# Kernel tuning notes

Hardware: AMD Instinct MI355X
Metric: run time of the kernel (lower is better)

The kernel has to match this reference:

```python
import jax, jax.numpy as jnp
import numpy as np

D_MODEL, N_HEADS, LATENT, ROPE = 4096, 128, 512, 64
HEAD_DIM = D_MODEL // N_HEADS  # 32
B, S = 2, 1024


def setup_inputs() -> dict:
    key = jax.random.key(0)
    ks = jax.random.split(key, 9)
    def w(k, i, o):
        return jax.random.normal(k, (i, o), dtype=jnp.float32) * (1.0 / np.sqrt(i))
    return {
        "x": jax.random.normal(ks[0], (B, S, D_MODEL), dtype=jnp.float32),
        "Wq_down": w(ks[1], D_MODEL, LATENT),
        "Wq_up": w(ks[2], LATENT, N_HEADS * HEAD_DIM),
        "Wq_rope": w(ks[3], D_MODEL, N_HEADS * ROPE),
        "Wkv_down": w(ks[4], D_MODEL, LATENT),
        "Wk_up": w(ks[5], LATENT, N_HEADS * HEAD_DIM),
        "Wv_up": w(ks[6], LATENT, N_HEADS * HEAD_DIM),
        "Wk_rope": w(ks[7], D_MODEL, ROPE),
        "Wo": w(ks[8], N_HEADS * HEAD_DIM, D_MODEL),
    }


def reference(x, Wq_down, Wq_up, Wq_rope, Wkv_down, Wk_up, Wv_up, Wk_rope, Wo):
    b, s, _ = x.shape
    # latent down-projections
    c_q = x @ Wq_down                                   # [B,S,latent]
    c_kv = x @ Wkv_down                                 # [B,S,latent]
    # up-projections, reshaped to per-head
    q_c = (c_q @ Wq_up).reshape(b, s, N_HEADS, HEAD_DIM)    # [B,S,H,Dh]
    q_r = (x @ Wq_rope).reshape(b, s, N_HEADS, ROPE)        # [B,S,H,Dr]
    k_c = (c_kv @ Wk_up).reshape(b, s, N_HEADS, HEAD_DIM)   # [B,S,H,Dh]
    v_c = (c_kv @ Wv_up).reshape(b, s, N_HEADS, HEAD_DIM)   # [B,S,H,Dh]
    k_r = x @ Wk_rope                                       # [B,S,Dr] shared over heads
    scale = jnp.asarray((HEAD_DIM + ROPE) ** 0.5, x.dtype)
    # scores = q.k with q=[q_c|q_r], k=[k_c|k_r(broadcast)] -> split the dot product
    scores = (jnp.einsum("bqhd,bkhd->bhqk", q_c, k_c)
              + jnp.einsum("bqhd,bkd->bhqk", q_r, k_r)) / scale  # [B,H,S,S]
    attn = jax.nn.softmax(scores, axis=-1)
    out = jnp.einsum("bhqk,bkhd->bqhd", attn, v_c)          # [B,S,H,Dh]
    out = out.reshape(b, s, N_HEADS * HEAD_DIM)
    return out @ Wo                                         # [B,S,d_model]
```

## Files before the change

kernel.cpp:

```cpp
#include <hip/hip_runtime.h>
#include <hip/hip_bf16.h>
#include <math.h>

#define D_MODEL 4096
#define N_HEADS 128
#define LATENT  512
#define ROPE_D  64
#define HEAD_D  32
#define BATCH   2
#define SEQ     1024
#define NTOK    (BATCH*SEQ)

typedef unsigned short u16;
typedef __attribute__((ext_vector_type(8))) short bf16x8;
typedef __attribute__((ext_vector_type(4))) float f32x4;

__device__ __forceinline__ u16 f2bf(float f) {
    union { float f; unsigned u; } v; v.f = f;
    unsigned r = (v.u + 0x7fffu + ((v.u >> 16) & 1u)) >> 16;
    return (u16)r;
}

__device__ __forceinline__ void gl_lds16(const u16* g, u16* l) {
    __builtin_amdgcn_global_load_lds(
        (const __attribute__((address_space(1))) unsigned int*)g,
        (__attribute__((address_space(3))) unsigned int*)l, 16, 0, 0);
}

__global__ __launch_bounds__(256)
void cast_x_kernel(const float* __restrict__ in, u16* __restrict__ out)
{
    size_t i = ((size_t)blockIdx.x * 256 + threadIdx.x) * 8;
    float4 a = *(const float4*)(in + i);
    float4 b = *(const float4*)(in + i + 4);
    u16 o[8] = {f2bf(a.x), f2bf(a.y), f2bf(a.z), f2bf(a.w),
                f2bf(b.x), f2bf(b.y), f2bf(b.z), f2bf(b.w)};
    *(bf16x8*)(out + i) = *(bf16x8*)o;
}

__global__ __launch_bounds__(256)
void castT_kernel(const float* __restrict__ W, u16* __restrict__ Wt,
                  int K, int N)
{
    __shared__ float tile[32][33];
    const int tid = threadIdx.x;
    const int j0 = blockIdx.x * 32;
    const int i0 = blockIdx.y * 32;
    #pragma unroll
    for (int it = 0; it < 4; ++it) {
        int e = tid + it * 256;
        int r = e >> 5, c = e & 31;
        tile[r][c] = (j0 + c < N) ? W[(size_t)(i0 + r) * N + j0 + c] : 0.f;
    }
    __syncthreads();
    #pragma unroll
    for (int it = 0; it < 4; ++it) {
        int e = tid + it * 256;
        int n = e >> 5, k = e & 31;
        Wt[(size_t)(j0 + n) * K + i0 + k] = f2bf(tile[k][n]);
    }
}

template<int OUTF32>
__global__ __launch_bounds__(256)
void gemm_bf16(const u16* __restrict__ A, const u16* __restrict__ Bt,
               void* __restrict__ Cout, int M, int N, int K,
               int lda, int ldb, int ldc)
{
    __shared__ __align__(16) u16 As[128 * 64];
    __shared__ __align__(16) u16 Bs[128 * 64];

    const int tid  = threadIdx.x;
    const int lane = tid & 63;
    const int wave = tid >> 6;
    const int wr = wave >> 1, wc = wave & 1;
    const int nwg  = gridDim.x * gridDim.y;
    const int orig = blockIdx.y * gridDim.x + blockIdx.x;
    const int swz  = (orig & 7) * (nwg >> 3) + (orig >> 3);
    const int bm = (swz / gridDim.x) * 128, bn = (swz % gridDim.x) * 128;
    const int l15 = lane & 15, lg = lane >> 4;

    f32x4 acc[4][4];
    #pragma unroll
    for (int i = 0; i < 4; ++i)
        #pragma unroll
        for (int j = 0; j < 4; ++j) acc[i][j] = (f32x4){0.f, 0.f, 0.f, 0.f};

    for (int kt = 0; kt < K; kt += 64) {
        __syncthreads();
        #pragma unroll
        for (int i = 0; i < 4; ++i) {
            int f = i * 256 + tid;
            int row = f >> 3, c = f & 7;
            int sc = c ^ (row & 7);
            gl_lds16(A + (size_t)(bm + row) * lda + kt + sc * 8, As + f * 8);
        }
        #pragma unroll
        for (int i = 0; i < 4; ++i) {
            int f = i * 256 + tid;
            int row = f >> 3, c = f & 7;
            int sc = c ^ (row & 7);
            gl_lds16(Bt + (size_t)(bn + row) * ldb + kt + sc * 8, Bs + f * 8);
        }
        __syncthreads();

        #pragma unroll
        for (int t = 0; t < 2; ++t) {
            bf16x8 af[4], bf[4];
            #pragma unroll
            for (int fm = 0; fm < 4; ++fm) {
                int row = wr * 64 + fm * 16 + l15;
                int c = (t * 4 + lg) ^ (row & 7);
                af[fm] = *(const bf16x8*)(As + row * 64 + c * 8);
            }
            #pragma unroll
            for (int fn = 0; fn < 4; ++fn) {
                int row = wc * 64 + fn * 16 + l15;
                int c = (t * 4 + lg) ^ (row & 7);
                bf[fn] = *(const bf16x8*)(Bs + row * 64 + c * 8);
            }
            #pragma unroll
            for (int fm = 0; fm < 4; ++fm)
                #pragma unroll
                for (int fn = 0; fn < 4; ++fn)
                    acc[fm][fn] = __builtin_amdgcn_mfma_f32_16x16x32_bf16(
                        af[fm], bf[fn], acc[fm][fn], 0, 0, 0);
        }
    }

    #pragma unroll
    for (int fm = 0; fm < 4; ++fm)
        #pragma unroll
        for (int fn = 0; fn < 4; ++fn)
            #pragma unroll
            for (int ri = 0; ri < 4; ++ri) {
                int row = bm + wr * 64 + fm * 16 + 4 * lg + ri;
                int col = bn + wc * 64 + fn * 16 + l15;
                if (col < N) {
                    float v = acc[fm][fn][ri];
                    if (OUTF32) ((float*)Cout)[(size_t)row * ldc + col] = v;
                    else        ((u16*)Cout)[(size_t)row * ldc + col] = f2bf(v);
                }
            }
}

__global__ __launch_bounds__(256)
void vtrans_kernel(const u16* __restrict__ vc, u16* __restrict__ vt)
{
    __shared__ __align__(16) u16 tile[64][72];
    const int tid = threadIdx.x;
    const int c0 = blockIdx.x * 64;
    const int s0 = blockIdx.y * 64;
    const int b  = blockIdx.z;
    #pragma unroll
    for (int it = 0; it < 2; ++it) {
        int e = it * 256 + tid;
        int r = e >> 3, c8 = e & 7;
        *(bf16x8*)&tile[r][c8 * 8] =
            *(const bf16x8*)(vc + (size_t)(b * SEQ + s0 + r) * 8192 + c0 + c8 * 8);
    }
    __syncthreads();
    #pragma unroll
    for (int it = 0; it < 2; ++it) {
        int e = it * 256 + tid;
        int d = e >> 3, c8 = e & 7;
        u16 o[8];
        #pragma unroll
        for (int j = 0; j < 8; ++j) o[j] = tile[c8 * 8 + j][d];
        *(bf16x8*)(vt + (size_t)(b * D_MODEL + c0 + d) * SEQ + s0 + c8 * 8) = *(bf16x8*)o;
    }
}

__global__ __launch_bounds__(256)
void attn_kernel(const u16* __restrict__ q_c, const u16* __restrict__ q_r,
                 const u16* __restrict__ k_c, const u16* __restrict__ k_r,
                 const u16* __restrict__ vt,  u16* __restrict__ attn_out)
{
    __shared__ __align__(16) u16 s_kc[2][64 * 32];
    __shared__ __align__(16) u16 s_kr[2][64 * 64];
    __shared__ __align__(16) u16 s_vt[2][32 * 64];
    __shared__ __align__(16) u16 s_p[4][16 * 64];

    const int tid  = threadIdx.x;
    const int lane = tid & 63;
    const int w    = tid >> 6;
    const int l15  = lane & 15, lg = lane >> 4;
    const int q0 = blockIdx.x * 64;
    const int h  = blockIdx.y;
    const int b  = blockIdx.z;
    const size_t bS = (size_t)b * SEQ;
    const int hc = h * HEAD_D;
    const float c2 = 0.1020620726159658f * 1.44269504088896f;

    const int qrow = q0 + w * 16 + l15;
    const bf16x8 qf0 = *(const bf16x8*)(q_c + (bS + qrow) * 4096 + hc + lg * 8);
    const bf16x8 qf1 = *(const bf16x8*)(q_r + (bS + qrow) * 9344 + h * ROPE_D + lg * 8);
    const bf16x8 qf2 = *(const bf16x8*)(q_r + (bS + qrow) * 9344 + h * ROPE_D + 32 + lg * 8);

    float m2 = -1e30f, lsum = 0.f;
    f32x4 oacc[2];
    oacc[0] = (f32x4){0.f, 0.f, 0.f, 0.f};
    oacc[1] = (f32x4){0.f, 0.f, 0.f, 0.f};

    auto stage = [&](int buf, int k0) {
        { int f = tid, r = f >> 2, c = f & 3;
          gl_lds16(k_c + (bS + k0 + r) * 8192 + hc + ((c ^ (r & 3)) << 3),
                   &s_kc[buf][f * 8]); }
        #pragma unroll
        for (int it = 0; it < 2; ++it) {
          int f = it * 256 + tid, r = f >> 3, c = f & 7;
          gl_lds16(k_r + (bS + k0 + r) * 9344 + ((c ^ (r & 7)) << 3),
                   &s_kr[buf][f * 8]); }
        { int f = tid, d = f >> 3, c = f & 7;
          gl_lds16(vt + ((size_t)b * D_MODEL + hc + d) * SEQ + k0 + ((c ^ (d & 7)) << 3),
                   &s_vt[buf][f * 8]); }
    };

    stage(0, 0);
    __syncthreads();

    int cur = 0;
    for (int t = 0; t < SEQ / 64; ++t) {
        if (t + 1 < SEQ / 64) stage(cur ^ 1, (t + 1) * 64);

        f32x4 sc[4];
        #pragma unroll
        for (int fc = 0; fc < 4; ++fc) sc[fc] = (f32x4){0.f, 0.f, 0.f, 0.f};
        __builtin_amdgcn_s_setprio(1);
        #pragma unroll
        for (int fc = 0; fc < 4; ++fc) {
            int row = fc * 16 + l15;
            bf16x8 kb = *(const bf16x8*)&s_kc[cur][row * 32 + ((lg ^ (row & 3)) << 3)];
            sc[fc] = __builtin_amdgcn_mfma_f32_16x16x32_bf16(kb, qf0, sc[fc], 0, 0, 0);
        }
        #pragma unroll
        for (int tt = 0; tt < 2; ++tt) {
            bf16x8 qf = tt ? qf2 : qf1;
            #pragma unroll
            for (int fc = 0; fc < 4; ++fc) {
                int row = fc * 16 + l15;
                bf16x8 kb = *(const bf16x8*)&s_kr[cur][row * 64 + (((tt * 4 + lg) ^ (row & 7)) << 3)];
                sc[fc] = __builtin_amdgcn_mfma_f32_16x16x32_bf16(kb, qf, sc[fc], 0, 0, 0);
            }
        }
        __builtin_amdgcn_s_setprio(0);

        float tmx = sc[0][0];
        #pragma unroll
        for (int fc = 0; fc < 4; ++fc)
            #pragma unroll
            for (int ri = 0; ri < 4; ++ri)
                tmx = fmaxf(tmx, sc[fc][ri]);
        tmx = fmaxf(tmx, __shfl_xor(tmx, 16));
        tmx = fmaxf(tmx, __shfl_xor(tmx, 32));
        float tl2 = tmx * c2;
        if (!__all(tl2 <= m2 + 8.f)) {
            float mn = fmaxf(m2, tl2);
            float corr = exp2f(m2 - mn);
            m2 = mn;
            lsum *= corr;
            #pragma unroll
            for (int ri = 0; ri < 4; ++ri) {
                float cr = __shfl(corr, 4 * lg + ri);
                oacc[0][ri] *= cr; oacc[1][ri] *= cr;
            }
        }
        float rs = 0.f;
        unsigned pk0[4], pk1[4];
        #pragma unroll
        for (int fc = 0; fc < 4; ++fc) {
            float p0 = exp2f(fmaf(sc[fc][0], c2, -m2));
            float p1 = exp2f(fmaf(sc[fc][1], c2, -m2));
            float p2 = exp2f(fmaf(sc[fc][2], c2, -m2));
            float p3 = exp2f(fmaf(sc[fc][3], c2, -m2));
            rs += (p0 + p1) + (p2 + p3);
            asm("v_cvt_pk_bf16_f32 %0, %1, %2" : "=v"(pk0[fc]) : "v"(p0), "v"(p1));
            asm("v_cvt_pk_bf16_f32 %0, %1, %2" : "=v"(pk1[fc]) : "v"(p2), "v"(p3));
        }
        rs += __shfl_xor(rs, 16);
        rs += __shfl_xor(rs, 32);
        lsum += rs;
        #pragma unroll
        for (int fc = 0; fc < 4; ++fc) {
            int ch = (2 * fc + (lg >> 1)) ^ (l15 & 7);
            *(uint2*)&s_p[w][l15 * 64 + ch * 8 + 4 * (lg & 1)] =
                make_uint2(pk0[fc], pk1[fc]);
        }

        __builtin_amdgcn_s_setprio(1);
        #pragma unroll
        for (int t2 = 0; t2 < 2; ++t2) {
            bf16x8 pa = *(const bf16x8*)&s_p[w][l15 * 64 + (((t2 * 4 + lg) ^ (l15 & 7)) << 3)];
            #pragma unroll
            for (int fd = 0; fd < 2; ++fd) {
                int row = fd * 16 + l15;
                bf16x8 vb = *(const bf16x8*)&s_vt[cur][row * 64 + (((t2 * 4 + lg) ^ (row & 7)) << 3)];
                oacc[fd] = __builtin_amdgcn_mfma_f32_16x16x32_bf16(pa, vb, oacc[fd], 0, 0, 0);
            }
        }
        __builtin_amdgcn_s_setprio(0);

        __syncthreads();
        cur ^= 1;
    }

    #pragma unroll
    for (int ri = 0; ri < 4; ++ri) {
        float ls = __shfl(lsum, 4 * lg + ri);
        float inv = 1.f / ls;
        int row = q0 + w * 16 + 4 * lg + ri;
        attn_out[(bS + row) * 4096 + hc + l15]      = f2bf(oacc[0][ri] * inv);
        attn_out[(bS + row) * 4096 + hc + 16 + l15] = f2bf(oacc[1][ri] * inv);
    }
}

extern "C" void kernel_launch(void* const* d_in, const int* in_sizes, int n_in,
                              void* d_out, int out_size, void* d_ws, size_t ws_size,
                              hipStream_t stream)
{
    (void)in_sizes; (void)n_in; (void)out_size; (void)ws_size;

    const float* x        = (const float*)d_in[0];
    const float* Wq_down  = (const float*)d_in[1];
    const float* Wq_up    = (const float*)d_in[2];
    const float* Wq_rope  = (const float*)d_in[3];
    const float* Wkv_down = (const float*)d_in[4];
    const float* Wk_up    = (const float*)d_in[5];
    const float* Wv_up    = (const float*)d_in[6];
    const float* Wk_rope  = (const float*)d_in[7];
    const float* Wo       = (const float*)d_in[8];

    u16* ws   = (u16*)d_ws;
    u16* xb   = ws;
    u16* BigT = xb + (size_t)8388608;
    u16* UpT  = BigT + (size_t)38273024;
    u16* WuqT = UpT + (size_t)4194304;
    u16* C_big= WuqT + (size_t)2097152;
    u16* C2   = C_big + (size_t)19136512;
    u16* WoT  = BigT;
    u16* vt   = BigT + (size_t)16777216;
    u16* q_c  = BigT + (size_t)25165824;
    u16* attn_out = xb;

    dim3 blk(256);

    hipMemsetAsync(BigT + (size_t)9280 * 4096, 0, (size_t)64 * 4096 * 2, stream);
    hipLaunchKernelGGL(cast_x_kernel, dim3(4096), blk, 0, stream, x, xb);
    hipLaunchKernelGGL(castT_kernel, dim3(256, 128), blk, 0, stream, Wq_rope, BigT, 4096, 8192);
    hipLaunchKernelGGL(castT_kernel, dim3(16, 128), blk, 0, stream, Wq_down, BigT + (size_t)8192 * 4096, 4096, 512);
    hipLaunchKernelGGL(castT_kernel, dim3(16, 128), blk, 0, stream, Wkv_down, BigT + (size_t)8704 * 4096, 4096, 512);
    hipLaunchKernelGGL(castT_kernel, dim3(2, 128), blk, 0, stream, Wk_rope, BigT + (size_t)9216 * 4096, 4096, 64);
    hipLaunchKernelGGL(castT_kernel, dim3(128, 16), blk, 0, stream, Wk_up, UpT, 512, 4096);
    hipLaunchKernelGGL(castT_kernel, dim3(128, 16), blk, 0, stream, Wv_up, UpT + (size_t)4096 * 512, 512, 4096);
    hipLaunchKernelGGL(castT_kernel, dim3(128, 16), blk, 0, stream, Wq_up, WuqT, 512, 4096);

    gemm_bf16<0><<<dim3(73, 16), blk, 0, stream>>>(xb, BigT, C_big, NTOK, 9344, 4096, 4096, 4096, 9344);
    hipLaunchKernelGGL(castT_kernel, dim3(128, 128), blk, 0, stream, Wo, WoT, 4096, 4096);
    gemm_bf16<0><<<dim3(64, 16), blk, 0, stream>>>(C_big + 8704, UpT, C2, NTOK, 8192, 512, 9344, 512, 8192);
    gemm_bf16<0><<<dim3(32, 16), blk, 0, stream>>>(C_big + 8192, WuqT, q_c, NTOK, 4096, 512, 9344, 512, 4096);
    hipLaunchKernelGGL(vtrans_kernel, dim3(64, 16, 2), blk, 0, stream, C2 + 4096, vt);
    hipLaunchKernelGGL(attn_kernel, dim3(16, 128, 2), blk, 0, stream,
                       q_c, C_big, C2, C_big + 9216, vt, attn_out);
    gemm_bf16<1><<<dim3(32, 16), blk, 0, stream>>>(attn_out, WoT, d_out, NTOK, 4096, 4096, 4096, 4096, 4096);
}
```

Before: 594.8 us.

## Replace GEMM with 256-row tiles, 4-stage LDS pipeline and 512 threads

Replaces the single-buffered 128x128 bf16 GEMM with a templated 256xBN kernel that uses 8 waves and a 4-deep ring of LDS buffers with K-step 32. Each loop iteration issues the next stage's global-to-LDS loads and waits on them with explicit vmcnt counts, so loads overlap the MFMA work. It also raises wave priority around the MFMA block and enlarges the per-wave tile to increase data reuse. In exchange it needs more LDS and registers, lowering occupancy. Grids get coarser, and the padded weight region and its zero-memset are enlarged to cover the 256-wide N tiles.

```diff
diff --git a/kernel.cpp b/kernel.cpp
--- a/kernel.cpp
+++ b/kernel.cpp
@@ -61,83 +61,110 @@
     }
 }
 
-template<int OUTF32>
-__global__ __launch_bounds__(256)
-void gemm_bf16(const u16* __restrict__ A, const u16* __restrict__ Bt,
-               void* __restrict__ Cout, int M, int N, int K,
-               int lda, int ldb, int ldc)
-{
-    __shared__ __align__(16) u16 As[128 * 64];
-    __shared__ __align__(16) u16 Bs[128 * 64];
+template<int BN_, int OUTF32>
+__global__ __launch_bounds__(512)
+void gemm256(const u16* __restrict__ A, const u16* __restrict__ Bt,
+             void* __restrict__ Cout, int M, int N, int K,
+             int lda, int ldb, int ldc)
+{
+    constexpr int WN   = BN_ / 4;
+    constexpr int NFR  = WN / 16;
+    constexpr int BUFE = 8192 + BN_ * 32;
+
+    extern __shared__ __align__(16) u16 lds[];
 
     const int tid  = threadIdx.x;
     const int lane = tid & 63;
     const int wave = tid >> 6;
-    const int wr = wave >> 1, wc = wave & 1;
+    const int wr = wave >> 2, wc = wave & 3;
+    const int l15 = lane & 15, lg = lane >> 4;
+
     const int nwg  = gridDim.x * gridDim.y;
     const int orig = blockIdx.y * gridDim.x + blockIdx.x;
     const int swz  = (orig & 7) * (nwg >> 3) + (orig >> 3);
-    const int bm = (swz / gridDim.x) * 128, bn = (swz % gridDim.x) * 128;
-    const int l15 = lane & 15, lg = lane >> 4;
-
-    f32x4 acc[4][4];
-    #pragma unroll
-    for (int i = 0; i < 4; ++i)
-        #pragma unroll
-        for (int j = 0; j < 4; ++j) acc[i][j] = (f32x4){0.f, 0.f, 0.f, 0.f};
-
-    for (int kt = 0; kt < K; kt += 64) {
-        __syncthreads();
-        #pragma unroll
-        for (int i = 0; i < 4; ++i) {
-            int f = i * 256 + tid;
-            int row = f >> 3, c = f & 7;
-            int sc = c ^ (row & 7);
-            gl_lds16(A + (size_t)(bm + row) * lda + kt + sc * 8, As + f * 8);
-        }
-        #pragma unroll
-        for (int i = 0; i < 4; ++i) {
-            int f = i * 256 + tid;
-            int row = f >> 3, c = f & 7;
-            int sc = c ^ (row & 7);
-            gl_lds16(Bt + (size_t)(bn + row) * ldb + kt + sc * 8, Bs + f * 8);
-        }
-        __syncthreads();
-
-        #pragma unroll
-        for (int t = 0; t < 2; ++t) {
-            bf16x8 af[4], bf[4];
-            #pragma unroll
-            for (int fm = 0; fm < 4; ++fm) {
-                int row = wr * 64 + fm * 16 + l15;
-                int c = (t * 4 + lg) ^ (row & 7);
-                af[fm] = *(const bf16x8*)(As + row * 64 + c * 8);
-            }
-            #pragma unroll
-            for (int fn = 0; fn < 4; ++fn) {
-                int row = wc * 64 + fn * 16 + l15;
-                int c = (t * 4 + lg) ^ (row & 7);
-                bf[fn] = *(const bf16x8*)(Bs + row * 64 + c * 8);
-            }
-            #pragma unroll
-            for (int fm = 0; fm < 4; ++fm)
-                #pragma unroll
-                for (int fn = 0; fn < 4; ++fn)
-                    acc[fm][fn] = __builtin_amdgcn_mfma_f32_16x16x32_bf16(
-                        af[fm], bf[fn], acc[fm][fn], 0, 0, 0);
-        }
-    }
-
-    #pragma unroll
-    for (int fm = 0; fm < 4; ++fm)
-        #pragma unroll
-        for (int fn = 0; fn < 4; ++fn)
+    const int bm = (swz / gridDim.x) * 256, bn = (swz % gridDim.x) * BN_;
+
+    const int NT = K >> 5;
+
+    auto stage = [&](int t) {
+        const int buf = t & 3;
+        u16* bA = lds + buf * BUFE;
+        u16* bB = bA + 8192;
+        const int kt = t * 32;
+        #pragma unroll
+        for (int it = 0; it < 2; ++it) {
+            int f = it * 512 + tid;
+            int row = f >> 2, c = f & 3;
+            int sc = (c ^ (row >> 1)) & 3;
+            gl_lds16(A + (size_t)(bm + row) * lda + kt + sc * 8, bA + f * 8);
+        }
+        #pragma unroll
+        for (int it = 0; it < BN_ / 128; ++it) {
+            int f = it * 512 + tid;
+            int row = f >> 2, c = f & 3;
+            int sc = (c ^ (row >> 1)) & 3;
+            gl_lds16(Bt + (size_t)(bn + row) * ldb + kt + sc * 8, bB + f * 8);
+        }
+    };
+
+    f32x4 acc[8][NFR];
+    #pragma unroll
+    for (int m = 0; m < 8; ++m)
+        #pragma unroll
+        for (int n = 0; n < NFR; ++n) acc[m][n] = (f32x4){0.f, 0.f, 0.f, 0.f};
+
+    stage(0); stage(1); stage(2);
+
+    for (int t = 0; t < NT; ++t) {
+        const int rem = NT - 1 - t;
+        if constexpr (BN_ == 256) {
+            if (rem >= 2)      asm volatile("s_waitcnt vmcnt(8)" ::: "memory");
+            else if (rem == 1) asm volatile("s_waitcnt vmcnt(4)" ::: "memory");
+            else               asm volatile("s_waitcnt vmcnt(0)" ::: "memory");
+        } else {
+            if (rem >= 2)      asm volatile("s_waitcnt vmcnt(6)" ::: "memory");
+            else if (rem == 1) asm volatile("s_waitcnt vmcnt(3)" ::: "memory");
+            else               asm volatile("s_waitcnt vmcnt(0)" ::: "memory");
+        }
+        __builtin_amdgcn_s_barrier();
+        asm volatile("" ::: "memory");
+
+        if (t + 3 < NT) stage(t + 3);
+
+        const u16* bA = lds + (t & 3) * BUFE;
+        const u16* bB = bA + 8192;
+
+        bf16x8 af[8], bfr[NFR];
+        #pragma unroll
+        for (int m = 0; m < 8; ++m) {
+            int row = wr * 128 + m * 16 + l15;
+            af[m] = *(const bf16x8*)(bA + row * 32 + (((lg ^ (row >> 1)) & 3) << 3));
+        }
+        #pragma unroll
+        for (int n = 0; n < NFR; ++n) {
+            int row = wc * WN + n * 16 + l15;
+            bfr[n] = *(const bf16x8*)(bB + row * 32 + (((lg ^ (row >> 1)) & 3) << 3));
+        }
+        __builtin_amdgcn_s_setprio(1);
+        #pragma unroll
+        for (int m = 0; m < 8; ++m)
+            #pragma unroll
+            for (int n = 0; n < NFR; ++n)
+                acc[m][n] = __builtin_amdgcn_mfma_f32_16x16x32_bf16(
+                    af[m], bfr[n], acc[m][n], 0, 0, 0);
+        __builtin_amdgcn_s_setprio(0);
+    }
+
+    #pragma unroll
+    for (int m = 0; m < 8; ++m)
+        #pragma unroll
+        for (int n = 0; n < NFR; ++n)
             #pragma unroll
             for (int ri = 0; ri < 4; ++ri) {
-                int row = bm + wr * 64 + fm * 16 + 4 * lg + ri;
-                int col = bn + wc * 64 + fn * 16 + l15;
+                int row = bm + wr * 128 + m * 16 + 4 * lg + ri;
+                int col = bn + wc * WN + n * 16 + l15;
                 if (col < N) {
-                    float v = acc[fm][fn][ri];
+                    float v = acc[m][n][ri];
                     if (OUTF32) ((float*)Cout)[(size_t)row * ldc + col] = v;
                     else        ((u16*)Cout)[(size_t)row * ldc + col] = f2bf(v);
                 }
@@ -333,7 +360,7 @@
     u16* ws   = (u16*)d_ws;
     u16* xb   = ws;
     u16* BigT = xb + (size_t)8388608;
-    u16* UpT  = BigT + (size_t)38273024;
+    u16* UpT  = BigT + (size_t)38797312;
     u16* WuqT = UpT + (size_t)4194304;
     u16* C_big= WuqT + (size_t)2097152;
     u16* C2   = C_big + (size_t)19136512;
@@ -344,7 +371,14 @@
 
     dim3 blk(256);
 
-    hipMemsetAsync(BigT + (size_t)9280 * 4096, 0, (size_t)64 * 4096 * 2, stream);
+    (void)hipFuncSetAttribute((const void*)&gemm256<256,0>,
+                              hipFuncAttributeMaxDynamicSharedMemorySize, 131072);
+    (void)hipFuncSetAttribute((const void*)&gemm256<128,0>,
+                              hipFuncAttributeMaxDynamicSharedMemorySize, 98304);
+    (void)hipFuncSetAttribute((const void*)&gemm256<128,1>,
+                              hipFuncAttributeMaxDynamicSharedMemorySize, 98304);
+
+    hipMemsetAsync(BigT + (size_t)9280 * 4096, 0, (size_t)192 * 4096 * 2, stream);
     hipLaunchKernelGGL(cast_x_kernel, dim3(4096), blk, 0, stream, x, xb);
     hipLaunchKernelGGL(castT_kernel, dim3(256, 128), blk, 0, stream, Wq_rope, BigT, 4096, 8192);
     hipLaunchKernelGGL(castT_kernel, dim3(16, 128), blk, 0, stream, Wq_down, BigT + (size_t)8192 * 4096, 4096, 512);
@@ -354,12 +388,16 @@
     hipLaunchKernelGGL(castT_kernel, dim3(128, 16), blk, 0, stream, Wv_up, UpT + (size_t)4096 * 512, 512, 4096);
     hipLaunchKernelGGL(castT_kernel, dim3(128, 16), blk, 0, stream, Wq_up, WuqT, 512, 4096);
 
-    gemm_bf16<0><<<dim3(73, 16), blk, 0, stream>>>(xb, BigT, C_big, NTOK, 9344, 4096, 4096, 4096, 9344);
+    gemm256<256,0><<<dim3(37, 8), dim3(512), 131072, stream>>>(
+        xb, BigT, C_big, NTOK, 9344, 4096, 4096, 4096, 9344);
     hipLaunchKernelGGL(castT_kernel, dim3(128, 128), blk, 0, stream, Wo, WoT, 4096, 4096);
-    gemm_bf16<0><<<dim3(64, 16), blk, 0, stream>>>(C_big + 8704, UpT, C2, NTOK, 8192, 512, 9344, 512, 8192);
-    gemm_bf16<0><<<dim3(32, 16), blk, 0, stream>>>(C_big + 8192, WuqT, q_c, NTOK, 4096, 512, 9344, 512, 4096);
+    gemm256<256,0><<<dim3(32, 8), dim3(512), 131072, stream>>>(
+        C_big + 8704, UpT, C2, NTOK, 8192, 512, 9344, 512, 8192);
+    gemm256<128,0><<<dim3(32, 8), dim3(512), 98304, stream>>>(
+        C_big + 8192, WuqT, q_c, NTOK, 4096, 512, 9344, 512, 4096);
     hipLaunchKernelGGL(vtrans_kernel, dim3(64, 16, 2), blk, 0, stream, C2 + 4096, vt);
     hipLaunchKernelGGL(attn_kernel, dim3(16, 128, 2), blk, 0, stream,
                        q_c, C_big, C2, C_big + 9216, vt, attn_out);
-    gemm_bf16<1><<<dim3(32, 16), blk, 0, stream>>>(attn_out, WoT, d_out, NTOK, 4096, 4096, 4096, 4096, 4096);
-}
+    gemm256<128,1><<<dim3(32, 8), dim3(512), 98304, stream>>>(
+        attn_out, WoT, d_out, NTOK, 4096, 4096, 4096, 4096, 4096);
+}
```

Measured after the change: 604.9 us. Within noise of the previous version (+1.7%).
